# Kernel optimization log

Hardware: AMD Instinct MI355X
Metric: run time of the kernel (lower is better)

Reference implementation:

```python
import jax, jax.numpy as jnp
import numpy as np
from jax import lax

EPS = 1e-5
ALPHA = 100.0

def leaky_relu(x):
    return jnp.where(x >= 0, x, 0.2 * x)

def instance_norm(x):
    # per-sample, per-channel over (H, W), affine=False, eps=1e-5
    m = jnp.mean(x, axis=(2, 3), keepdims=True)
    v = jnp.var(x, axis=(2, 3), keepdims=True)
    return (x - m) / jnp.sqrt(v + EPS)

def conv2d(x, W, b, stride=1):
    y = lax.conv_general_dilated(x, W, (stride, stride), 'VALID',
                                 dimension_numbers=('NCHW', 'OIHW', 'NCHW'))
    return y + b[None, :, None, None]

def leaky_conv(x, W, b, pad, stride):
    # ReflectionPad2d(pad) -> Conv2d(pad=0) -> InstanceNorm -> LeakyReLU(0.2)
    if pad > 0:
        x = jnp.pad(x, ((0, 0), (0, 0), (pad, pad), (pad, pad)), mode='reflect')
    y = conv2d(x, W, b, stride)
    return leaky_relu(instance_norm(y))

def up2x_align_corners(x):
    # nn.UpsamplingBilinear2d(scale_factor=2) == bilinear with align_corners=True
    n, c, H, W = x.shape
    def coords(S):
        pos = jnp.arange(2 * S, dtype=x.dtype) * (S - 1) / (2 * S - 1)
        i0 = jnp.floor(pos).astype(jnp.int32)
        i1 = jnp.minimum(i0 + 1, S - 1)
        return i0, i1, pos - i0
    i0, i1, fh = coords(H)
    x = x[:, :, i0, :] * (1 - fh)[None, None, :, None] + x[:, :, i1, :] * fh[None, None, :, None]
    j0, j1, fw = coords(W)
    x = x[:, :, :, j0] * (1 - fw) + x[:, :, :, j1] * fw
    return x

def upsample_block(x, W, b):
    x = up2x_align_corners(x)
    # Conv2d(3,3,k=3,s=1,p=1) uses ZERO padding (plain nn.Conv2d padding arg)
    x = jnp.pad(x, ((0, 0), (0, 0), (1, 1), (1, 1)))
    return leaky_relu(instance_norm(conv2d(x, W, b)))

def cal_correlation(fa, fb, alpha):
    n, c, h, w = fa.shape
    fa = fa - jnp.mean(fa, axis=(2, 3), keepdims=True)
    fb = fb - jnp.mean(fb, axis=(2, 3), keepdims=True)
    fa = fa.reshape(n, c, h * w)
    fb = fb.reshape(n, c, h * w)
    fa = fa / (jnp.linalg.norm(fa, axis=1, keepdims=True) + EPS)
    fb = fb / (jnp.linalg.norm(fb, axis=1, keepdims=True) + EPS)
    energy = jnp.einsum('ncp,ncq->npq', fb, fa) * alpha  # [n, hw_b, hw_a]
    return jax.nn.softmax(energy, axis=1)

def setup_inputs() -> dict:
    key = jax.random.key(0)
    ks = jax.random.split(key, 16)
    C = 256
    d = {
        'fa_raw': jax.random.normal(ks[0], (2, C, 64, 64), jnp.float32),
        'fb_raw': jax.random.normal(ks[1], (2, C, 64, 64), jnp.float32),
        'fc_raw': jax.random.normal(ks[2], (2, 3, 256, 256), jnp.float32),
        'Wa': jax.random.normal(ks[3], (C // 4, C, 1, 1), jnp.float32) * 0.05,
        'ba': jnp.zeros((C // 4,), jnp.float32),
        'Wb': jax.random.normal(ks[4], (C // 4, C, 1, 1), jnp.float32) * 0.05,
        'bb': jnp.zeros((C // 4,), jnp.float32),
        'Wc1': jax.random.normal(ks[5], (3, 3, 3, 3), jnp.float32) * 0.2,
        'bc1': jnp.zeros((3,), jnp.float32),
        'Wc2': jax.random.normal(ks[6], (3, 3, 3, 3), jnp.float32) * 0.2,
        'bc2': jnp.zeros((3,), jnp.float32),
        'Wu1': jax.random.normal(ks[7], (3, 3, 3, 3), jnp.float32) * 0.2,
        'bu1': jnp.zeros((3,), jnp.float32),
        'Wu2': jax.random.normal(ks[8], (3, 3, 3, 3), jnp.float32) * 0.2,
        'bu2': jnp.zeros((3,), jnp.float32),
    }
    return d

def reference(fa_raw, fb_raw, fc_raw, Wa, ba, Wb, bb, Wc1, bc1, Wc2, bc2, Wu1, bu1, Wu2, bu2):
    fa = leaky_conv(fa_raw, Wa, ba, pad=0, stride=1)          # [n, 64, 64, 64]
    fb = leaky_conv(fb_raw, Wb, bb, pad=0, stride=1)
    fc = leaky_conv(fc_raw, Wc1, bc1, pad=1, stride=2)        # [n, 3, 128, 128]
    fc = leaky_conv(fc, Wc2, bc2, pad=1, stride=2)            # [n, 3, 64, 64]
    corr_ab_T = cal_correlation(fa, fb, ALPHA)                # [n, 4096, 4096]
    n, c, h, w = fc.shape
    fc_warp = jnp.einsum('ncp,npq->ncq', fc.reshape(n, c, h * w), corr_ab_T)
    fc_warp = fc_warp.reshape(n, c, h, w)
    fc_warp = upsample_block(fc_warp, Wu1, bu1)               # [n, 3, 128, 128]
    fc_warp = upsample_block(fc_warp, Wu2, bu2)               # [n, 3, 256, 256]
    return fc_warp, corr_ab_T
```

## Files before the change

### kernel.cpp

```cpp
#include <hip/hip_runtime.h>
#include <math.h>

#define EPS 1e-5f

typedef short short8 __attribute__((ext_vector_type(8)));
typedef __bf16 bf16x8 __attribute__((ext_vector_type(8)));
typedef float f32x4  __attribute__((ext_vector_type(4)));

__device__ __forceinline__ float lrelu(float x){ return x >= 0.f ? x : 0.2f*x; }

__device__ __forceinline__ short f2bf_s(float x){
    unsigned u = __float_as_uint(x);
    unsigned r = (u + 0x7FFFu + ((u >> 16) & 1u)) >> 16;
    return (short)r;
}
__device__ __forceinline__ float bfs2f(short h){
    return __uint_as_float(((unsigned)(unsigned short)h) << 16);
}

__device__ __forceinline__ f32x4 mfma16(bf16x8 a, bf16x8 b, f32x4 c){
    return __builtin_amdgcn_mfma_f32_16x16x32_bf16(a, b, c, 0, 0, 0);
}

__global__ __launch_bounds__(256,2) void feat_conv(
    const float* __restrict__ fa_raw, const float* __restrict__ fb_raw,
    const float* __restrict__ Wa, const float* __restrict__ Wb,
    const float* __restrict__ ba, const float* __restrict__ bb,
    float* __restrict__ Y, float* __restrict__ FSUM)
{
    __shared__ float wS[256*65];
    __shared__ float xS[16*64];

    int blk = blockIdx.x;
    int pch = blk & 63, n = (blk>>6)&1, side = blk>>7;
    int p0 = pch*64;
    const float* x    = (side ? fb_raw : fa_raw) + (size_t)n*256*4096 + p0;
    const float* W    = side ? Wb : Wa;
    const float* bias = side ? bb : ba;
    int tid = threadIdx.x;

    #pragma unroll
    for (int it=0; it<64; it++){
        int idx = it*256 + tid;
        int co = idx >> 8, ci = idx & 255;
        wS[ci*65 + co] = W[idx];
    }

    int pl = tid & 63, cog = tid >> 6;
    float acc[16];
    #pragma unroll
    for (int j=0;j<16;j++) acc[j] = 0.f;

    for (int cb=0; cb<16; cb++){
        __syncthreads();
        #pragma unroll
        for (int it=0; it<4; it++){
            int idx = it*256 + tid;
            int cl = idx >> 6, pp = idx & 63;
            xS[idx] = x[(size_t)(cb*16+cl)*4096 + pp];
        }
        __syncthreads();
        #pragma unroll
        for (int cl=0; cl<16; cl++){
            float xr = xS[cl*64 + pl];
            const float* wr = &wS[(cb*16+cl)*65 + cog*16];
            #pragma unroll
            for (int j=0;j<16;j++) acc[j] = fmaf(xr, wr[j], acc[j]);
        }
    }

    int pair = side*2 + n;
    #pragma unroll
    for (int j=0;j<16;j++){
        acc[j] += bias[cog*16+j];
        float v = acc[j], v2 = v*v;
        #pragma unroll
        for (int off=1; off<64; off<<=1){
            v  += __shfl_xor(v,  off);
            v2 += __shfl_xor(v2, off);
        }
        if (pl == 0){
            atomicAdd(&FSUM[(pair*64 + cog*16 + j)*2],   v);
            atomicAdd(&FSUM[(pair*64 + cog*16 + j)*2+1], v2);
        }
    }

    float* yr = Y + ((size_t)pair*4096 + p0 + pl)*64 + cog*16;
    #pragma unroll
    for (int j4=0;j4<4;j4++)
        *(float4*)(yr + j4*4) = make_float4(acc[j4*4],acc[j4*4+1],acc[j4*4+2],acc[j4*4+3]);
}

__global__ void fstats_kernel(const float* __restrict__ FSUM, float* __restrict__ FST)
{
    int ch = threadIdx.x;
    float m = FSUM[ch*2] * (1.f/4096.f);
    float v = FSUM[ch*2+1] * (1.f/4096.f) - m*m;
    FST[ch*2]   = m;
    FST[ch*2+1] = rsqrtf(v + EPS);
}

__global__ __launch_bounds__(256) void feat_apply(
    float* __restrict__ Y, const float* __restrict__ FST, float* __restrict__ M2SUM)
{
    __shared__ float red[256];
    int tid = threadIdx.x;
    size_t base = (size_t)blockIdx.x*4096;
    int pair = (int)(base >> 18);
    int co = tid & 63;
    float m   = FST[(pair*64+co)*2];
    float inv = FST[(pair*64+co)*2+1];
    float asum = 0.f;
    #pragma unroll
    for (int it=0; it<16; it++){
        size_t idx = base + it*256 + tid;
        float y2 = lrelu((Y[idx]-m)*inv);
        Y[idx] = y2;
        asum += y2;
    }
    red[tid] = asum; __syncthreads();
    if (tid < 64)
        atomicAdd(&M2SUM[pair*64 + tid], red[tid]+red[tid+64]+red[tid+128]+red[tid+192]);
}

__global__ void feat_finish(float* __restrict__ Y, const float* __restrict__ M2SUM)
{
    int r = blockIdx.x*256 + threadIdx.x;
    int pair = r >> 12;
    const float4* m4 = (const float4*)(M2SUM + pair*64);
    float4* r4 = (float4*)(Y + (size_t)r*64);
    float s = 0.f;
    float4 v[16];
    #pragma unroll
    for (int i=0;i<16;i++){
        float4 t = r4[i], mm = m4[i];
        t.x -= mm.x*(1.f/4096.f); t.y -= mm.y*(1.f/4096.f);
        t.z -= mm.z*(1.f/4096.f); t.w -= mm.w*(1.f/4096.f);
        v[i] = t;
        s += t.x*t.x + t.y*t.y + t.z*t.z + t.w*t.w;
    }
    float inv = 1.f/(sqrtf(s)+EPS);
    #pragma unroll
    for (int i=0;i<16;i++){ v[i].x*=inv; v[i].y*=inv; v[i].z*=inv; v[i].w*=inv; r4[i]=v[i]; }
}

template<int STRIDE, bool REFLECT>
__global__ void conv3_kernel(const float* __restrict__ in_, int H, int Wd,
                             const float* __restrict__ wgt,
                             const float* __restrict__ bias,
                             float* __restrict__ out, float* __restrict__ sums)
{
    int oH = (H-1)/STRIDE + 1, oW = (Wd-1)/STRIDE + 1;
    int tid = threadIdx.x;
    size_t idx = (size_t)blockIdx.x*256 + tid;
    int ow = (int)(idx % oW); size_t t = idx / oW;
    int oh = (int)(t % oH); t /= oH;
    int co = (int)(t % 3); int n = (int)(t/3);
    float w[27];
    #pragma unroll
    for (int i=0;i<27;i++) w[i] = wgt[co*27 + i];
    float acc = bias[co];
    #pragma unroll
    for (int ci=0;ci<3;ci++){
        size_t base = ((size_t)(n*3+ci))*H*Wd;
        #pragma unroll
        for (int kh=0;kh<3;kh++){
            int ih = oh*STRIDE + kh - 1;
            if (REFLECT) ih = ih<0 ? -ih : (ih>=H ? 2*H-2-ih : ih);
            #pragma unroll
            for (int kw=0;kw<3;kw++){
                int iw = ow*STRIDE + kw - 1;
                if (REFLECT) iw = iw<0 ? -iw : (iw>=Wd ? 2*Wd-2-iw : iw);
                bool ok = REFLECT || (ih>=0 && ih<H && iw>=0 && iw<Wd);
                if (ok) acc += w[(ci*3+kh)*3+kw] * in_[base + (size_t)ih*Wd + iw];
            }
        }
    }
    out[idx] = acc;
    __shared__ float red[256];
    red[tid] = acc; __syncthreads();
    for (int o=128;o>0;o>>=1){ if(tid<o) red[tid]+=red[tid+o]; __syncthreads(); }
    float blockSum = red[0]; __syncthreads();
    red[tid] = acc*acc; __syncthreads();
    for (int o=128;o>0;o>>=1){ if(tid<o) red[tid]+=red[tid+o]; __syncthreads(); }
    if (tid==0){
        int pair = n*3+co;
        atomicAdd(&sums[pair*2],   blockSum);
        atomicAdd(&sums[pair*2+1], red[0]);
    }
}

__global__ void instats_kernel(const float* __restrict__ sums, float* __restrict__ mstats, float cntInv)
{
    int i = threadIdx.x;
    if (i < 6){
        float m = sums[i*2]*cntInv;
        float v = sums[i*2+1]*cntInv - m*m;
        mstats[i*2]   = m;
        mstats[i*2+1] = rsqrtf(v + EPS);
    }
}

__global__ void inapply_kernel(const float* __restrict__ in, const float* __restrict__ mstats,
                               int planeSize, float* __restrict__ out)
{
    size_t idx = (size_t)blockIdx.x*256 + threadIdx.x;
    int pair = (int)(idx / planeSize);
    float m = mstats[pair*2], inv = mstats[pair*2+1];
    out[idx] = lrelu((in[idx]-m)*inv);
}

__global__ void up2x_kernel(const float* __restrict__ in, int H, int Wd, float* __restrict__ out)
{
    int oH = 2*H, oW = 2*Wd;
    size_t idx = (size_t)blockIdx.x*256 + threadIdx.x;
    int ow = (int)(idx % oW); size_t t = idx/oW;
    int oh = (int)(t % oH); int pl = (int)(t/oH);
    float ph = (float)oh * (float)(H-1)  / (float)(oH-1);
    float pw = (float)ow * (float)(Wd-1) / (float)(oW-1);
    int i0 = (int)ph; int i1 = min(i0+1, H-1); float fh = ph - (float)i0;
    int j0 = (int)pw; int j1 = min(j0+1, Wd-1); float fw = pw - (float)j0;
    const float* p = in + (size_t)pl*H*Wd;
    float v00=p[(size_t)i0*Wd+j0], v01=p[(size_t)i0*Wd+j1];
    float v10=p[(size_t)i1*Wd+j0], v11=p[(size_t)i1*Wd+j1];
    float v0 = v00 + (v01-v00)*fw;
    float v1 = v10 + (v11-v10)*fw;
    out[idx] = v0 + (v1-v0)*fh;
}

template<int PASS>
__global__ __launch_bounds__(256,2) void corr_mfma(
    const float* __restrict__ faT, const float* __restrict__ fbT,
    float* __restrict__ corr, float* __restrict__ SSUM,
    const float* __restrict__ INVS,
    const float* __restrict__ fc, float* __restrict__ WARP)
{
    __shared__ short lds[32768];

    int blk = blockIdx.x;
    int qb = blk & 31, pb = (blk >> 5) & 31, n = blk >> 10;
    int tid = threadIdx.x;

    const float* faB = faT + ((size_t)n*4096 + (size_t)qb*128)*64;
    const float* fbB = fbT + ((size_t)n*4096 + (size_t)pb*128)*64;
    #pragma unroll
    for (int it=0; it<8; it++){
        int cid = it*256 + tid;
        int side = cid >> 10;
        int idx  = cid & 1023;
        int r = idx & 15, c = (idx>>4)&7, g = idx>>7;
        int grow = g*16 + r;
        const float* src = (side ? faB : fbB) + grow*64 + c*8;
        float4 x0 = *(const float4*)src;
        float4 x1 = *(const float4*)(src+4);
        float xs[8] = {x0.x,x0.y,x0.z,x0.w,x1.x,x1.y,x1.z,x1.w};
        short8 h, l;
        #pragma unroll
        for (int j=0;j<8;j++){
            short hh = f2bf_s(xs[j]);
            h[j] = hh;
            l[j] = f2bf_s(xs[j] - bfs2f(hh));
        }
        int base16 = side*16384;
        *(short8*)(lds + base16 + idx*8)        = h;
        *(short8*)(lds + base16 + 8192 + idx*8) = l;
    }
    __syncthreads();

    int wave = tid >> 6, lane = tid & 63;
    int wp = wave >> 1, wq = wave & 1;
    int quad = lane >> 4, l16 = lane & 15;

    f32x4 acc[4][4];
    #pragma unroll
    for (int pt=0;pt<4;pt++)
        #pragma unroll
        for (int qt=0;qt<4;qt++)
            acc[pt][qt] = (f32x4){0.f,0.f,0.f,0.f};

    #pragma unroll
    for (int kc=0;kc<2;kc++){
        int cc = kc*4 + quad;
        bf16x8 Ah[4], Al[4], Bh[4], Bl[4];
        #pragma unroll
        for (int t4=0;t4<4;t4++){
            int offA = (((wp*4+t4)*8 + cc)*16 + l16)*8;
            Ah[t4] = (bf16x8)(*(const short8*)(lds + offA));
            Al[t4] = (bf16x8)(*(const short8*)(lds + 8192 + offA));
            int offB = 16384 + (((wq*4+t4)*8 + cc)*16 + l16)*8;
            Bh[t4] = (bf16x8)(*(const short8*)(lds + offB));
            Bl[t4] = (bf16x8)(*(const short8*)(lds + 8192 + offB));
        }
        #pragma unroll
        for (int pt=0;pt<4;pt++)
            #pragma unroll
            for (int qt=0;qt<4;qt++){
                acc[pt][qt] = mfma16(Ah[pt], Bh[qt], acc[pt][qt]);
                acc[pt][qt] = mfma16(Ah[pt], Bl[qt], acc[pt][qt]);
                acc[pt][qt] = mfma16(Al[pt], Bh[qt], acc[pt][qt]);
            }
    }

    if (PASS == 0){
        float colsum[4] = {0.f,0.f,0.f,0.f};
        #pragma unroll
        for (int pt=0;pt<4;pt++)
            #pragma unroll
            for (int qt=0;qt<4;qt++)
                #pragma unroll
                for (int i=0;i<4;i++)
                    colsum[qt] += __expf(fmaf(acc[pt][qt][i], 100.f, -64.f));
        #pragma unroll
        for (int qt=0;qt<4;qt++){
            float v = colsum[qt];
            v += __shfl_xor(v, 16);
            v += __shfl_xor(v, 32);
            if (lane < 16)
                atomicAdd(&SSUM[n*4096 + qb*128 + wq*64 + qt*16 + lane], v);
        }
    } else {
        float inv4[4];
        int qoff = n*4096 + qb*128 + wq*64 + l16;
        #pragma unroll
        for (int qt=0;qt<4;qt++) inv4[qt] = INVS[qoff + qt*16];
        float wa0[4]={0,0,0,0}, wa1[4]={0,0,0,0}, wa2[4]={0,0,0,0};
        const float* fcb = fc + (size_t)n*12288;
        float* corrN = corr + (size_t)n*4096*4096;
        #pragma unroll
        for (int pt=0;pt<4;pt++){
            #pragma unroll
            for (int i=0;i<4;i++){
                int p = pb*128 + wp*64 + pt*16 + quad*4 + i;
                float f0 = fcb[p], f1 = fcb[4096+p], f2 = fcb[8192+p];
                float* rowp = corrN + (size_t)p*4096 + qb*128 + wq*64 + l16;
                #pragma unroll
                for (int qt=0;qt<4;qt++){
                    float u = __expf(fmaf(acc[pt][qt][i], 100.f, -64.f)) * inv4[qt];
                    __builtin_nontemporal_store(u, &rowp[qt*16]);
                    wa0[qt] += f0*u; wa1[qt] += f1*u; wa2[qt] += f2*u;
                }
            }
        }
        #pragma unroll
        for (int qt=0;qt<4;qt++){
            float v0 = wa0[qt], v1 = wa1[qt], v2 = wa2[qt];
            v0 += __shfl_xor(v0,16); v0 += __shfl_xor(v0,32);
            v1 += __shfl_xor(v1,16); v1 += __shfl_xor(v1,32);
            v2 += __shfl_xor(v2,16); v2 += __shfl_xor(v2,32);
            if (lane < 16){
                int q = qb*128 + wq*64 + qt*16 + lane;
                atomicAdd(&WARP[(size_t)n*12288 +        q], v0);
                atomicAdd(&WARP[(size_t)n*12288 + 4096 + q], v1);
                atomicAdd(&WARP[(size_t)n*12288 + 8192 + q], v2);
            }
        }
    }
}

__global__ void inv_kernel(const float* __restrict__ SSUM, float* __restrict__ INVS)
{
    int i = blockIdx.x*256 + threadIdx.x;
    INVS[i] = 1.f / SSUM[i];
}

extern "C" void kernel_launch(void* const* d_in, const int* in_sizes, int n_in,
                              void* d_out, int out_size, void* d_ws, size_t ws_size,
                              hipStream_t stream)
{
    const float* fa_raw = (const float*)d_in[0];
    const float* fb_raw = (const float*)d_in[1];
    const float* fc_raw = (const float*)d_in[2];
    const float* Wa  = (const float*)d_in[3];
    const float* ba  = (const float*)d_in[4];
    const float* Wb  = (const float*)d_in[5];
    const float* bb  = (const float*)d_in[6];
    const float* Wc1 = (const float*)d_in[7];
    const float* bc1 = (const float*)d_in[8];
    const float* Wc2 = (const float*)d_in[9];
    const float* bc2 = (const float*)d_in[10];
    const float* Wu1 = (const float*)d_in[11];
    const float* bu1 = (const float*)d_in[12];
    const float* Wu2 = (const float*)d_in[13];
    const float* bu2 = (const float*)d_in[14];

    float* ws    = (float*)d_ws;
    float* FEAT  = ws;
    float* CONV1 = FEAT  + 1048576;
    float* FC64  = CONV1 + 98304;
    float* UP1   = FC64  + 24576;
    float* CONV2 = UP1   + 98304;
    float* UP2   = CONV2 + 98304;
    float* CONV3 = UP2   + 393216;
    float* SSUM  = CONV3 + 393216;
    float* SUMS  = SSUM  + 8192;
    float* FSUM  = SUMS  + 48;
    float* M2SUM = FSUM  + 512;
    float* WARP  = M2SUM + 256;
    float* MST   = WARP  + 24576;
    float* FST   = MST   + 48;
    float* INVS  = FST   + 512;

    float* faT = FEAT;
    float* fbT = FEAT + 524288;

    float* out_fc   = (float*)d_out;
    float* out_corr = out_fc + 393216;

    hipMemsetAsync(SSUM, 0, (size_t)(8192 + 48 + 512 + 256 + 24576)*sizeof(float), stream);

    feat_conv<<<256,256,0,stream>>>(fa_raw, fb_raw, Wa, Wb, ba, bb, FEAT, FSUM);
    fstats_kernel<<<1,256,0,stream>>>(FSUM, FST);
    feat_apply<<<512,256,0,stream>>>(FEAT, FST, M2SUM);
    feat_finish<<<64,256,0,stream>>>(FEAT, M2SUM);

    conv3_kernel<2,true><<<384,256,0,stream>>>(fc_raw, 256,256, Wc1, bc1, CONV1, SUMS+0);
    instats_kernel<<<1,64,0,stream>>>(SUMS+0,  MST+0,  1.f/16384.f);
    inapply_kernel<<<384,256,0,stream>>>(CONV1, MST+0,  16384, CONV1);
    conv3_kernel<2,true><<<96,256,0,stream>>>(CONV1, 128,128, Wc2, bc2, FC64, SUMS+12);
    instats_kernel<<<1,64,0,stream>>>(SUMS+12, MST+12, 1.f/4096.f);
    inapply_kernel<<<96,256,0,stream>>>(FC64, MST+12, 4096, FC64);

    corr_mfma<0><<<2048,256,0,stream>>>(faT, fbT, out_corr, SSUM, INVS, FC64, WARP);
    inv_kernel<<<32,256,0,stream>>>(SSUM, INVS);
    corr_mfma<1><<<2048,256,0,stream>>>(faT, fbT, out_corr, SSUM, INVS, FC64, WARP);

    up2x_kernel<<<384,256,0,stream>>>(WARP, 64,64, UP1);
    conv3_kernel<1,false><<<384,256,0,stream>>>(UP1, 128,128, Wu1, bu1, CONV2, SUMS+24);
    instats_kernel<<<1,64,0,stream>>>(SUMS+24, MST+24, 1.f/16384.f);
    inapply_kernel<<<384,256,0,stream>>>(CONV2, MST+24, 16384, CONV2);

    up2x_kernel<<<1536,256,0,stream>>>(CONV2, 128,128, UP2);
    conv3_kernel<1,false><<<1536,256,0,stream>>>(UP2, 256,256, Wu2, bu2, CONV3, SUMS+36);
    instats_kernel<<<1,64,0,stream>>>(SUMS+36, MST+36, 1.f/65536.f);
    inapply_kernel<<<1536,256,0,stream>>>(CONV3, MST+36, 65536, out_fc);
}
```

Baseline: 399.8 us.

## Prepack bf16 hi/lo features, fuse upsample into conv, drop stats kernels

feat_finish now writes the normalized features directly as pre-split bf16 hi/lo tiles in the LDS layout. Both correlation passes can then copy tiles straight into shared memory instead of re-converting fp32 per block. The bilinear upsample is folded into the following 3x3 conv, removing the intermediate upsampled buffers. The small stats, inverse-sum and instats kernels are removed, with their work recomputed inline in the consumer kernels, which cuts launches and global round trips. The trade-offs are extra workspace for the packed tiles and redundant upsample interpolation per conv tap.

```diff
diff --git a/kernel.cpp b/kernel.cpp
--- a/kernel.cpp
+++ b/kernel.cpp
@@ -91,25 +91,18 @@
         *(float4*)(yr + j4*4) = make_float4(acc[j4*4],acc[j4*4+1],acc[j4*4+2],acc[j4*4+3]);
 }
 
-__global__ void fstats_kernel(const float* __restrict__ FSUM, float* __restrict__ FST)
-{
-    int ch = threadIdx.x;
-    float m = FSUM[ch*2] * (1.f/4096.f);
-    float v = FSUM[ch*2+1] * (1.f/4096.f) - m*m;
-    FST[ch*2]   = m;
-    FST[ch*2+1] = rsqrtf(v + EPS);
-}
-
 __global__ __launch_bounds__(256) void feat_apply(
-    float* __restrict__ Y, const float* __restrict__ FST, float* __restrict__ M2SUM)
+    float* __restrict__ Y, const float* __restrict__ FSUM, float* __restrict__ M2SUM)
 {
     __shared__ float red[256];
     int tid = threadIdx.x;
     size_t base = (size_t)blockIdx.x*4096;
     int pair = (int)(base >> 18);
     int co = tid & 63;
-    float m   = FST[(pair*64+co)*2];
-    float inv = FST[(pair*64+co)*2+1];
+    int ch = pair*64 + co;
+    float m   = FSUM[ch*2]   * (1.f/4096.f);
+    float var = FSUM[ch*2+1] * (1.f/4096.f) - m*m;
+    float inv = rsqrtf(var + EPS);
     float asum = 0.f;
     #pragma unroll
     for (int it=0; it<16; it++){
@@ -123,12 +116,14 @@
         atomicAdd(&M2SUM[pair*64 + tid], red[tid]+red[tid+64]+red[tid+128]+red[tid+192]);
 }
 
-__global__ void feat_finish(float* __restrict__ Y, const float* __restrict__ M2SUM)
+__global__ void feat_finish(const float* __restrict__ Y, const float* __restrict__ M2SUM,
+                            short* __restrict__ PK)
 {
     int r = blockIdx.x*256 + threadIdx.x;
     int pair = r >> 12;
+    int p = r & 4095;
     const float4* m4 = (const float4*)(M2SUM + pair*64);
-    float4* r4 = (float4*)(Y + (size_t)r*64);
+    const float4* r4 = (const float4*)(Y + (size_t)r*64);
     float s = 0.f;
     float4 v[16];
     #pragma unroll
@@ -141,7 +136,25 @@
     }
     float inv = 1.f/(sqrtf(s)+EPS);
     #pragma unroll
-    for (int i=0;i<16;i++){ v[i].x*=inv; v[i].y*=inv; v[i].z*=inv; v[i].w*=inv; r4[i]=v[i]; }
+    for (int i=0;i<16;i++){ v[i].x*=inv; v[i].y*=inv; v[i].z*=inv; v[i].w*=inv; }
+
+    int qb = p >> 7, rr = p & 127, g = rr >> 4, rl = rr & 15;
+    short* blk = PK + (((size_t)pair*32 + qb) << 14);
+    #pragma unroll
+    for (int c=0;c<8;c++){
+        float x[8] = {v[2*c].x, v[2*c].y, v[2*c].z, v[2*c].w,
+                      v[2*c+1].x, v[2*c+1].y, v[2*c+1].z, v[2*c+1].w};
+        short8 h, l;
+        #pragma unroll
+        for (int j=0;j<8;j++){
+            short hh = f2bf_s(x[j]);
+            h[j] = hh;
+            l[j] = f2bf_s(x[j] - bfs2f(hh));
+        }
+        int idx = g*128 + c*16 + rl;
+        *(short8*)(blk + idx*8)        = h;
+        *(short8*)(blk + 8192 + idx*8) = l;
+    }
 }
 
 template<int STRIDE, bool REFLECT>
@@ -190,49 +203,90 @@
     }
 }
 
-__global__ void instats_kernel(const float* __restrict__ sums, float* __restrict__ mstats, float cntInv)
-{
-    int i = threadIdx.x;
-    if (i < 6){
-        float m = sums[i*2]*cntInv;
-        float v = sums[i*2+1]*cntInv - m*m;
-        mstats[i*2]   = m;
-        mstats[i*2+1] = rsqrtf(v + EPS);
-    }
-}
-
-__global__ void inapply_kernel(const float* __restrict__ in, const float* __restrict__ mstats,
-                               int planeSize, float* __restrict__ out)
+template<int H>
+__global__ __launch_bounds__(256) void upconv3_kernel(
+    const float* __restrict__ in_, const float* __restrict__ wgt,
+    const float* __restrict__ bias, float* __restrict__ out,
+    float* __restrict__ sums)
+{
+    const int oH = 2*H;
+    int tid = threadIdx.x;
+    size_t idx = (size_t)blockIdx.x*256 + tid;
+    int ow = (int)(idx % oH); size_t t = idx / oH;
+    int oh = (int)(t % oH); t /= oH;
+    int co = (int)(t % 3); int n = (int)(t/3);
+
+    float w[27];
+    #pragma unroll
+    for (int i=0;i<27;i++) w[i] = wgt[co*27 + i];
+
+    int i0[3], i1[3], j0[3], j1[3];
+    float fh[3], fw[3];
+    bool vh[3], vw[3];
+    #pragma unroll
+    for (int k=0;k<3;k++){
+        int ih = oh + k - 1;
+        vh[k] = (ih>=0 && ih<oH);
+        int ihc = vh[k] ? ih : 0;
+        float ph = (float)ihc * (float)(H-1) / (float)(oH-1);
+        i0[k] = (int)ph; i1[k] = min(i0[k]+1, H-1); fh[k] = ph - (float)i0[k];
+        int iw = ow + k - 1;
+        vw[k] = (iw>=0 && iw<oH);
+        int iwc = vw[k] ? iw : 0;
+        float pw = (float)iwc * (float)(H-1) / (float)(oH-1);
+        j0[k] = (int)pw; j1[k] = min(j0[k]+1, H-1); fw[k] = pw - (float)j0[k];
+    }
+
+    float acc = bias[co];
+    #pragma unroll
+    for (int ci=0;ci<3;ci++){
+        const float* p = in_ + ((size_t)(n*3+ci))*H*H;
+        #pragma unroll
+        for (int kh=0;kh<3;kh++){
+            if (!vh[kh]) continue;
+            const float* r0 = p + (size_t)i0[kh]*H;
+            const float* r1 = p + (size_t)i1[kh]*H;
+            #pragma unroll
+            for (int kw=0;kw<3;kw++){
+                if (!vw[kw]) continue;
+                float v00=r0[j0[kw]], v01=r0[j1[kw]];
+                float v10=r1[j0[kw]], v11=r1[j1[kw]];
+                float v0 = v00 + (v01-v00)*fw[kw];
+                float v1 = v10 + (v11-v10)*fw[kw];
+                float u  = v0 + (v1-v0)*fh[kh];
+                acc += w[(ci*3+kh)*3+kw] * u;
+            }
+        }
+    }
+    out[idx] = acc;
+    __shared__ float red[256];
+    red[tid] = acc; __syncthreads();
+    for (int o=128;o>0;o>>=1){ if(tid<o) red[tid]+=red[tid+o]; __syncthreads(); }
+    float blockSum = red[0]; __syncthreads();
+    red[tid] = acc*acc; __syncthreads();
+    for (int o=128;o>0;o>>=1){ if(tid<o) red[tid]+=red[tid+o]; __syncthreads(); }
+    if (tid==0){
+        int pair = n*3+co;
+        atomicAdd(&sums[pair*2],   blockSum);
+        atomicAdd(&sums[pair*2+1], red[0]);
+    }
+}
+
+__global__ void inapply_kernel(const float* __restrict__ in, const float* __restrict__ sums,
+                               int planeSize, float cntInv, float* __restrict__ out)
 {
     size_t idx = (size_t)blockIdx.x*256 + threadIdx.x;
     int pair = (int)(idx / planeSize);
-    float m = mstats[pair*2], inv = mstats[pair*2+1];
+    float m = sums[pair*2]*cntInv;
+    float v = sums[pair*2+1]*cntInv - m*m;
+    float inv = rsqrtf(v + EPS);
     out[idx] = lrelu((in[idx]-m)*inv);
-}
-
-__global__ void up2x_kernel(const float* __restrict__ in, int H, int Wd, float* __restrict__ out)
-{
-    int oH = 2*H, oW = 2*Wd;
-    size_t idx = (size_t)blockIdx.x*256 + threadIdx.x;
-    int ow = (int)(idx % oW); size_t t = idx/oW;
-    int oh = (int)(t % oH); int pl = (int)(t/oH);
-    float ph = (float)oh * (float)(H-1)  / (float)(oH-1);
-    float pw = (float)ow * (float)(Wd-1) / (float)(oW-1);
-    int i0 = (int)ph; int i1 = min(i0+1, H-1); float fh = ph - (float)i0;
-    int j0 = (int)pw; int j1 = min(j0+1, Wd-1); float fw = pw - (float)j0;
-    const float* p = in + (size_t)pl*H*Wd;
-    float v00=p[(size_t)i0*Wd+j0], v01=p[(size_t)i0*Wd+j1];
-    float v10=p[(size_t)i1*Wd+j0], v11=p[(size_t)i1*Wd+j1];
-    float v0 = v00 + (v01-v00)*fw;
-    float v1 = v10 + (v11-v10)*fw;
-    out[idx] = v0 + (v1-v0)*fh;
 }
 
 template<int PASS>
 __global__ __launch_bounds__(256,2) void corr_mfma(
-    const float* __restrict__ faT, const float* __restrict__ fbT,
+    const short* __restrict__ PK,
     float* __restrict__ corr, float* __restrict__ SSUM,
-    const float* __restrict__ INVS,
     const float* __restrict__ fc, float* __restrict__ WARP)
 {
     __shared__ short lds[32768];
@@ -241,29 +295,15 @@
     int qb = blk & 31, pb = (blk >> 5) & 31, n = blk >> 10;
     int tid = threadIdx.x;
 
-    const float* faB = faT + ((size_t)n*4096 + (size_t)qb*128)*64;
-    const float* fbB = fbT + ((size_t)n*4096 + (size_t)pb*128)*64;
-    #pragma unroll
-    for (int it=0; it<8; it++){
+    const short* pkB = PK + (((size_t)(2+n)*32 + pb) << 14);
+    const short* pkA = PK + (((size_t)( n )*32 + qb) << 14);
+    #pragma unroll
+    for (int it=0; it<16; it++){
         int cid = it*256 + tid;
-        int side = cid >> 10;
-        int idx  = cid & 1023;
-        int r = idx & 15, c = (idx>>4)&7, g = idx>>7;
-        int grow = g*16 + r;
-        const float* src = (side ? faB : fbB) + grow*64 + c*8;
-        float4 x0 = *(const float4*)src;
-        float4 x1 = *(const float4*)(src+4);
-        float xs[8] = {x0.x,x0.y,x0.z,x0.w,x1.x,x1.y,x1.z,x1.w};
-        short8 h, l;
-        #pragma unroll
-        for (int j=0;j<8;j++){
-            short hh = f2bf_s(xs[j]);
-            h[j] = hh;
-            l[j] = f2bf_s(xs[j] - bfs2f(hh));
-        }
-        int base16 = side*16384;
-        *(short8*)(lds + base16 + idx*8)        = h;
-        *(short8*)(lds + base16 + 8192 + idx*8) = l;
+        int side = cid >> 11;
+        int off  = (cid & 2047)*8;
+        short8 vv = *(const short8*)((side ? pkA : pkB) + off);
+        *(short8*)(lds + side*16384 + off) = vv;
     }
     __syncthreads();
 
@@ -322,7 +362,7 @@
         float inv4[4];
         int qoff = n*4096 + qb*128 + wq*64 + l16;
         #pragma unroll
-        for (int qt=0;qt<4;qt++) inv4[qt] = INVS[qoff + qt*16];
+        for (int qt=0;qt<4;qt++) inv4[qt] = 1.f / SSUM[qoff + qt*16];
         float wa0[4]={0,0,0,0}, wa1[4]={0,0,0,0}, wa2[4]={0,0,0,0};
         const float* fcb = fc + (size_t)n*12288;
         float* corrN = corr + (size_t)n*4096*4096;
@@ -355,12 +395,6 @@
             }
         }
     }
-}
-
-__global__ void inv_kernel(const float* __restrict__ SSUM, float* __restrict__ INVS)
-{
-    int i = blockIdx.x*256 + threadIdx.x;
-    INVS[i] = 1.f / SSUM[i];
 }
 
 extern "C" void kernel_launch(void* const* d_in, const int* in_sizes, int n_in,
@@ -387,21 +421,14 @@
     float* FEAT  = ws;
     float* CONV1 = FEAT  + 1048576;
     float* FC64  = CONV1 + 98304;
-    float* UP1   = FC64  + 24576;
-    float* CONV2 = UP1   + 98304;
-    float* UP2   = CONV2 + 98304;
-    float* CONV3 = UP2   + 393216;
+    float* CONV2 = FC64  + 24576;
+    float* CONV3 = CONV2 + 98304;
     float* SSUM  = CONV3 + 393216;
     float* SUMS  = SSUM  + 8192;
     float* FSUM  = SUMS  + 48;
     float* M2SUM = FSUM  + 512;
     float* WARP  = M2SUM + 256;
-    float* MST   = WARP  + 24576;
-    float* FST   = MST   + 48;
-    float* INVS  = FST   + 512;
-
-    float* faT = FEAT;
-    float* fbT = FEAT + 524288;
+    short* PK    = (short*)(WARP + 24576);
 
     float* out_fc   = (float*)d_out;
     float* out_corr = out_fc + 393216;
@@ -409,28 +436,20 @@
     hipMemsetAsync(SSUM, 0, (size_t)(8192 + 48 + 512 + 256 + 24576)*sizeof(float), stream);
 
     feat_conv<<<256,256,0,stream>>>(fa_raw, fb_raw, Wa, Wb, ba, bb, FEAT, FSUM);
-    fstats_kernel<<<1,256,0,stream>>>(FSUM, FST);
-    feat_apply<<<512,256,0,stream>>>(FEAT, FST, M2SUM);
-    feat_finish<<<64,256,0,stream>>>(FEAT, M2SUM);
+    feat_apply<<<256,256,0,stream>>>(FEAT, FSUM, M2SUM);
+    feat_finish<<<64,256,0,stream>>>(FEAT, M2SUM, PK);
 
     conv3_kernel<2,true><<<384,256,0,stream>>>(fc_raw, 256,256, Wc1, bc1, CONV1, SUMS+0);
-    instats_kernel<<<1,64,0,stream>>>(SUMS+0,  MST+0,  1.f/16384.f);
-    inapply_kernel<<<384,256,0,stream>>>(CONV1, MST+0,  16384, CONV1);
+    inapply_kernel<<<384,256,0,stream>>>(CONV1, SUMS+0, 16384, 1.f/16384.f, CONV1);
     conv3_kernel<2,true><<<96,256,0,stream>>>(CONV1, 128,128, Wc2, bc2, FC64, SUMS+12);
-    instats_kernel<<<1,64,0,stream>>>(SUMS+12, MST+12, 1.f/4096.f);
-    inapply_kernel<<<96,256,0,stream>>>(FC64, MST+12, 4096, FC64);
-
-    corr_mfma<0><<<2048,256,0,stream>>>(faT, fbT, out_corr, SSUM, INVS, FC64, WARP);
-    inv_kernel<<<32,256,0,stream>>>(SSUM, INVS);
-    corr_mfma<1><<<2048,256,0,stream>>>(faT, fbT, out_corr, SSUM, INVS, FC64, WARP);
-
-    up2x_kernel<<<384,256,0,stream>>>(WARP, 64,64, UP1);
-    conv3_kernel<1,false><<<384,256,0,stream>>>(UP1, 128,128, Wu1, bu1, CONV2, SUMS+24);
-    instats_kernel<<<1,64,0,stream>>>(SUMS+24, MST+24, 1.f/16384.f);
-    inapply_kernel<<<384,256,0,stream>>>(CONV2, MST+24, 16384, CONV2);
-
-    up2x_kernel<<<1536,256,0,stream>>>(CONV2, 128,128, UP2);
-    conv3_kernel<1,false><<<1536,256,0,stream>>>(UP2, 256,256, Wu2, bu2, CONV3, SUMS+36);
-    instats_kernel<<<1,64,0,stream>>>(SUMS+36, MST+36, 1.f/65536.f);
-    inapply_kernel<<<1536,256,0,stream>>>(CONV3, MST+36, 65536, out_fc);
-}
+    inapply_kernel<<<96,256,0,stream>>>(FC64, SUMS+12, 4096, 1.f/4096.f, FC64);
+
+    corr_mfma<0><<<2048,256,0,stream>>>(PK, out_corr, SSUM, FC64, WARP);
+    corr_mfma<1><<<2048,256,0,stream>>>(PK, out_corr, SSUM, FC64, WARP);
+
+    upconv3_kernel<64><<<384,256,0,stream>>>(WARP, Wu1, bu1, CONV2, SUMS+24);
+    inapply_kernel<<<384,256,0,stream>>>(CONV2, SUMS+24, 16384, 1.f/16384.f, CONV2);
+
+    upconv3_kernel<128><<<1536,256,0,stream>>>(CONV2, Wu2, bu2, CONV3, SUMS+36);
+    inapply_kernel<<<1536,256,0,stream>>>(CONV3, SUMS+36, 65536, 1.f/65536.f, out_fc);
+}
```

New measurement: 365.3 us. 1.09x faster.
